# Kernel tuning notes

Measured on AMD Instinct MI355X. Metric: run time of the kernel, lower is better.

The kernel has to match this reference:

```python
import jax, jax.numpy as jnp
import numpy as np

N = 100000   # nodes
E = 800000   # edges
F_IN, H, C = 128, 128, 47
L = 3        # layers


def setup_inputs() -> dict:
    key = jax.random.key(0)
    ks = jax.random.split(key, 10)
    x = jax.random.normal(ks[0], (N, F_IN), dtype=jnp.float32)
    src = jax.random.randint(ks[1], (E,), 0, N, dtype=jnp.int32)
    dst = jax.random.randint(ks[2], (E,), 0, N, dtype=jnp.int32)
    w = jax.random.uniform(ks[3], (L, E), dtype=jnp.float32)
    W0 = jax.random.normal(ks[4], (F_IN, H), dtype=jnp.float32) * 0.05
    b0 = jnp.zeros((H,), jnp.float32)
    W1 = jax.random.normal(ks[5], (H, H), dtype=jnp.float32) * 0.05
    b1 = jnp.zeros((H,), jnp.float32)
    W2 = jax.random.normal(ks[6], (H, C), dtype=jnp.float32) * 0.05
    b2 = jnp.zeros((C,), jnp.float32)
    return {"x": x, "src": src, "dst": dst, "w": w,
            "W0": W0, "b0": b0, "W1": W1, "b1": b1, "W2": W2, "b2": b2}


def reference(x, src, dst, w, W0, b0, W1, b1, W2, b2):
    seg = lambda v, idx: jax.ops.segment_sum(v, idx, num_segments=N)
    ones = jnp.ones((src.shape[0],), x.dtype)
    # DGL GraphConv norm='both': structural degrees, clamped to >= 1
    inv_sqrt_out = jnp.maximum(seg(ones, src), 1.0) ** -0.5  # [N]
    inv_sqrt_in = jnp.maximum(seg(ones, dst), 1.0) ** -0.5   # [N]

    def gcn_layer(h, we, W, b):
        h = h * inv_sqrt_out[:, None]          # src normalization
        h = h @ W                               # linear (commutes with linear agg)
        m = h[src] * we[:, None]                # edge-weighted messages [E, d]
        agg = seg(m, dst)                       # scatter-add to dst [N, d]
        return agg * inv_sqrt_in[:, None] + b   # dst normalization + bias

    h = jax.nn.relu(gcn_layer(x, w[0], W0, b0))
    h = jax.nn.relu(gcn_layer(h, w[1], W1, b1))
    return gcn_layer(h, w[2], W2, b2)
```

## Files before the change

### kernel.cpp

```cpp
#include <hip/hip_runtime.h>


typedef short s16x8 __attribute__((ext_vector_type(8)));
typedef float f32x4 __attribute__((ext_vector_type(4)));

static constexpr int CAP = 24;

__device__ __forceinline__ unsigned short f2bf(float f) {
    unsigned int u = __float_as_uint(f);
    u += 0x7FFFu + ((u >> 16) & 1u);
    return (unsigned short)(u >> 16);
}
__device__ __forceinline__ float bf2f(unsigned short v) {
    return __uint_as_float((unsigned int)v << 16);
}

__global__ __launch_bounds__(256)
void pack_all(const float* __restrict__ W0, const float* __restrict__ W1,
              const float* __restrict__ W2, unsigned short* __restrict__ Wp) {
    int idx = blockIdx.x * 256 + threadIdx.x;
    if (idx < 32768) {
        const float* W = (idx < 16384) ? W0 : W1;
        unsigned short* D = Wp + ((idx < 16384) ? 0 : 16384);
        int i = idx & 16383;
        int k = i >> 7, col = i & 127;
        float v = W[k * 128 + col];
        int kk = k >> 5, kr = k & 31;
        int lane = ((kr >> 3) << 4) | (col & 15);
        int ct = col >> 4, j = kr & 7;
        D[(((kk * 8) + ct) * 64 + lane) * 8 + j] = f2bf(v);
    } else if (idx < 40960) {
        int i = idx - 32768;
        int k = i >> 6, col = i & 63;
        float v = (col < 47) ? W2[k * 47 + col] : 0.0f;
        int kk = k >> 5, kr = k & 31;
        int lane = ((kr >> 3) << 4) | (col & 15);
        int ct = col >> 4, j = kr & 7;
        (Wp + 32768)[(((kk * 4) + ct) * 64 + lane) * 8 + j] = f2bf(v);
    }
}

__global__ __launch_bounds__(256)
void mega_fill_gemm0(const int* __restrict__ src, const int* __restrict__ dst,
                     const float* __restrict__ w, int E,
                     int* __restrict__ dego, int* __restrict__ cursor,
                     float4* __restrict__ swb,
                     int* __restrict__ spill_cnt, int2* __restrict__ spill,
                     const float* __restrict__ x,
                     const unsigned short* __restrict__ Wp0,
                     unsigned short* __restrict__ y, int N, int gemm_blocks) {
    const int b = blockIdx.x;
    if (b % 3 == 2) {
        const int gb = b / 3;
        if (gb >= gemm_blocks) return;
        const int lane = threadIdx.x & 63;
        const int wid  = threadIdx.x >> 6;
        const int row0 = gb * 64 + wid * 16;
        const int kgrp = lane >> 4;
        const int c    = lane & 15;
        int ar = row0 + c;
        if (ar > N - 1) ar = N - 1;
        const float* xrow = &x[(size_t)ar * 128];

        f32x4 acc[8];
        #pragma unroll
        for (int ct = 0; ct < 8; ++ct) acc[ct] = {0.f, 0.f, 0.f, 0.f};

        #pragma unroll
        for (int kk = 0; kk < 4; ++kk) {
            float4 u0 = *(const float4*)&xrow[kk * 32 + kgrp * 8];
            float4 u1 = *(const float4*)&xrow[kk * 32 + kgrp * 8 + 4];
            s16x8 af;
            af[0] = (short)f2bf(u0.x); af[1] = (short)f2bf(u0.y);
            af[2] = (short)f2bf(u0.z); af[3] = (short)f2bf(u0.w);
            af[4] = (short)f2bf(u1.x); af[5] = (short)f2bf(u1.y);
            af[6] = (short)f2bf(u1.z); af[7] = (short)f2bf(u1.w);
            #pragma unroll
            for (int ct = 0; ct < 8; ++ct) {
                s16x8 bf = *(const s16x8*)&Wp0[((size_t)(kk * 8 + ct) * 64 + lane) * 8];
                acc[ct] = __builtin_amdgcn_mfma_f32_16x16x32_bf16(af, bf, acc[ct], 0, 0, 0);
            }
        }
        #pragma unroll
        for (int ct = 0; ct < 8; ++ct) {
            #pragma unroll
            for (int i = 0; i < 4; ++i) {
                int row = row0 + kgrp * 4 + i;
                if (row < N) y[(size_t)row * 128 + ct * 16 + c] = f2bf(acc[ct][i]);
            }
        }
    } else {
        const int fb = b - b / 3;
        int e = fb * 256 + (int)threadIdx.x;
        if (e >= E) return;
        int s = src[e];
        int d = dst[e];
        atomicAdd(&dego[s], 1);
        int pos = atomicAdd(&cursor[d], 1);
        if (pos < CAP) {
            swb[(size_t)d * CAP + pos] =
                make_float4(__int_as_float(s), w[e], w[E + e], w[2 * (size_t)E + e]);
        } else {
            int sp = atomicAdd(spill_cnt, 1);
            spill[sp] = make_int2(d, e);
        }
    }
}

template<int PC>
__global__ __launch_bounds__(256)
void gemm_direct(const unsigned short* __restrict__ h,
                 const unsigned short* __restrict__ Wp,
                 unsigned short* __restrict__ y, int N) {
    constexpr int CT = PC / 16;
    const int lane = threadIdx.x & 63;
    const int wid  = threadIdx.x >> 6;
    const int row0 = blockIdx.x * 64 + wid * 16;
    const int kgrp = lane >> 4;
    const int c    = lane & 15;

    int ar = row0 + c;
    if (ar > N - 1) ar = N - 1;
    const unsigned short* hrow = &h[(size_t)ar * 128 + kgrp * 8];

    f32x4 acc[CT];
    #pragma unroll
    for (int ct = 0; ct < CT; ++ct) acc[ct] = {0.f, 0.f, 0.f, 0.f};

    #pragma unroll
    for (int kk = 0; kk < 4; ++kk) {
        s16x8 af = *(const s16x8*)&hrow[kk * 32];
        #pragma unroll
        for (int ct = 0; ct < CT; ++ct) {
            s16x8 bf = *(const s16x8*)&Wp[((size_t)(kk * CT + ct) * 64 + lane) * 8];
            acc[ct] = __builtin_amdgcn_mfma_f32_16x16x32_bf16(af, bf, acc[ct], 0, 0, 0);
        }
    }

    #pragma unroll
    for (int ct = 0; ct < CT; ++ct) {
        #pragma unroll
        for (int i = 0; i < 4; ++i) {
            int row = row0 + kgrp * 4 + i;
            if (row < N) y[(size_t)row * PC + ct * 16 + c] = f2bf(acc[ct][i]);
        }
    }
}

template<int PC, int WSEL, bool FINAL>
__global__ __launch_bounds__(256)
void gather_w(const unsigned short* __restrict__ yb, const float4* __restrict__ swb,
              const int* __restrict__ degi, const int* __restrict__ dego,
              const int* __restrict__ spill_cnt, const int2* __restrict__ spill,
              const int* __restrict__ src, const float* __restrict__ wl,
              const float* __restrict__ b, void* __restrict__ outp, int N) {
    constexpr int TPN = PC / 4;
    constexpr int EPG = 64 / TPN;
    const int n = blockIdx.x * 4 + (threadIdx.x >> 6);
    if (n >= N) return;
    const int t    = threadIdx.x & 63;
    const int lane = t & (TPN - 1);
    const int g    = t / TPN;

    const ushort4* yv = (const ushort4*)yb;
    const float4* rec = swb + (size_t)n * CAP;
    const int dg  = degi[n];
    const int cnt = dg < CAP ? dg : CAP;

    float a0 = 0.f, a1 = 0.f, a2 = 0.f, a3 = 0.f;
    int p = g;

#define SELW(m) ((WSEL == 0) ? (m).y : (WSEL == 1) ? (m).z : (m).w)
#define EDGE_FMA(m, v) do {                                                   \
        int _s = __float_as_int((m).x);                                       \
        int _d = dego[_s]; if (_d < 1) _d = 1;                                \
        float _w = SELW(m) * rsqrtf((float)_d);                               \
        a0 = fmaf(bf2f((v).x), _w, a0);                                       \
        a1 = fmaf(bf2f((v).y), _w, a1);                                       \
        a2 = fmaf(bf2f((v).z), _w, a2);                                       \
        a3 = fmaf(bf2f((v).w), _w, a3);                                       \
    } while (0)

    for (; p + 3 * EPG < cnt; p += 4 * EPG) {
        float4 m0 = rec[p];
        float4 m1 = rec[p + EPG];
        float4 m2 = rec[p + 2 * EPG];
        float4 m3 = rec[p + 3 * EPG];
        ushort4 v0 = yv[(size_t)__float_as_int(m0.x) * TPN + lane];
        ushort4 v1 = yv[(size_t)__float_as_int(m1.x) * TPN + lane];
        ushort4 v2 = yv[(size_t)__float_as_int(m2.x) * TPN + lane];
        ushort4 v3 = yv[(size_t)__float_as_int(m3.x) * TPN + lane];
        EDGE_FMA(m0, v0); EDGE_FMA(m1, v1); EDGE_FMA(m2, v2); EDGE_FMA(m3, v3);
    }
    for (; p + EPG < cnt; p += 2 * EPG) {
        float4 m0 = rec[p];
        float4 m1 = rec[p + EPG];
        ushort4 v0 = yv[(size_t)__float_as_int(m0.x) * TPN + lane];
        ushort4 v1 = yv[(size_t)__float_as_int(m1.x) * TPN + lane];
        EDGE_FMA(m0, v0); EDGE_FMA(m1, v1);
    }
    if (p < cnt) {
        float4 m0 = rec[p];
        ushort4 v0 = yv[(size_t)__float_as_int(m0.x) * TPN + lane];
        EDGE_FMA(m0, v0);
    }
    if (dg > CAP && g == 0) {
        int sc = *spill_cnt;
        for (int i = 0; i < sc; ++i) {
            int2 sp = spill[i];
            if (sp.x == n) {
                int e = sp.y;
                int s0 = src[e];
                int d0 = dego[s0]; if (d0 < 1) d0 = 1;
                float w0 = wl[e] * rsqrtf((float)d0);
                ushort4 v0 = yv[(size_t)s0 * TPN + lane];
                a0 = fmaf(bf2f(v0.x), w0, a0);
                a1 = fmaf(bf2f(v0.y), w0, a1);
                a2 = fmaf(bf2f(v0.z), w0, a2);
                a3 = fmaf(bf2f(v0.w), w0, a3);
            }
        }
    }
#undef EDGE_FMA
#undef SELW

    #pragma unroll
    for (int m = TPN; m < 64; m <<= 1) {
        a0 += __shfl_xor(a0, m, 64);
        a1 += __shfl_xor(a1, m, 64);
        a2 += __shfl_xor(a2, m, 64);
        a3 += __shfl_xor(a3, m, 64);
    }
    if (g != 0) return;

    const float inv = rsqrtf((float)(dg < 1 ? 1 : dg));
    if (FINAL) {
        float* out = (float*)outp;
        const int c = lane * 4;
        float aa[4] = {a0, a1, a2, a3};
        #pragma unroll
        for (int j = 0; j < 4; ++j) {
            if (c + j < 47) out[(size_t)n * 47 + c + j] = fmaf(aa[j], inv, b[c + j]);
        }
    } else {
        unsigned short* out = (unsigned short*)outp;
        float4 bb = *(const float4*)&b[lane * 4];
        float4 v;
        v.x = fmaxf(fmaf(a0, inv, bb.x), 0.f);
        v.y = fmaxf(fmaf(a1, inv, bb.y), 0.f);
        v.z = fmaxf(fmaf(a2, inv, bb.z), 0.f);
        v.w = fmaxf(fmaf(a3, inv, bb.w), 0.f);
        ushort4 o;
        o.x = f2bf(v.x); o.y = f2bf(v.y); o.z = f2bf(v.z); o.w = f2bf(v.w);
        *(ushort4*)&out[(size_t)n * PC + lane * 4] = o;
    }
}

extern "C" void kernel_launch(void* const* d_in, const int* in_sizes, int n_in,
                              void* d_out, int out_size, void* d_ws, size_t ws_size,
                              hipStream_t stream) {
    const float* x   = (const float*)d_in[0];
    const int*   src = (const int*)d_in[1];
    const int*   dst = (const int*)d_in[2];
    const float* w   = (const float*)d_in[3];
    const float* W0  = (const float*)d_in[4];
    const float* b0  = (const float*)d_in[5];
    const float* W1  = (const float*)d_in[6];
    const float* b1  = (const float*)d_in[7];
    const float* W2  = (const float*)d_in[8];
    const float* b2  = (const float*)d_in[9];

    const int N = in_sizes[0] / 128;
    const int E = in_sizes[1];

    char* p = (char*)d_ws;
    unsigned short* xh = (unsigned short*)p; p += (size_t)N * 128 * sizeof(unsigned short);
    unsigned short* y  = (unsigned short*)p; p += (size_t)N * 128 * sizeof(unsigned short);
    float4* swb    = (float4*)p; p += (size_t)N * CAP * sizeof(float4);
    int2*   spill  = (int2*)p;   p += (size_t)E * sizeof(int2);
    unsigned short* Wp = (unsigned short*)p; p += (size_t)(16384 * 2 + 8192) * sizeof(unsigned short);
    int*   dego    = (int*)p;    p += (size_t)N * sizeof(int);
    int*   cursor  = (int*)p;    p += (size_t)N * sizeof(int);
    int*   spill_cnt = (int*)p;  p += 4 * sizeof(int);

    unsigned short* Wp1 = Wp + 16384;
    unsigned short* Wp2 = Wp + 32768;

    hipMemsetAsync(dego, 0, (2 * (size_t)N + 4) * sizeof(int), stream);
    pack_all<<<160, 256, 0, stream>>>(W0, W1, W2, Wp);

    const int gemm_blocks = (N + 63) / 64;
    const int fill_blocks = (E + 255) / 256;
    int grid = 3 * gemm_blocks;
    if (grid - grid / 3 < fill_blocks) grid = (3 * fill_blocks + 1) / 2 + 2;
    mega_fill_gemm0<<<grid, 256, 0, stream>>>(
        src, dst, w, E, dego, cursor, swb, spill_cnt, spill,
        x, Wp, y, N, gemm_blocks);

    const int gather_blocks = (N + 3) / 4;

    gather_w<128, 0, false><<<gather_blocks, 256, 0, stream>>>(
        y, swb, cursor, dego, spill_cnt, spill, src, w, b0, xh, N);

    gemm_direct<128><<<gemm_blocks, 256, 0, stream>>>(xh, Wp1, y, N);
    gather_w<128, 1, false><<<gather_blocks, 256, 0, stream>>>(
        y, swb, cursor, dego, spill_cnt, spill, src, w + E, b1, xh, N);

    gemm_direct<64><<<gemm_blocks, 256, 0, stream>>>(xh, Wp2, y, N);
    gather_w<64, 2, true><<<gather_blocks, 256, 0, stream>>>(
        y, swb, cursor, dego, spill_cnt, spill, src, w + 2 * (size_t)E, b2, d_out, N);
}
```

Before: 255.0 us.

## Fuse gather with next-layer GEMM via LDS; shrink edge records to (src, edge id)

Each layer's gather/aggregate is fused with the following layer's MFMA GEMM. Every block aggregates 64 destination rows into swizzled shared memory and then runs the GEMM from LDS, so the intermediate bf16 activations never make a round trip through global memory and two launches go away. Edge records shrink from float4 (src plus three weights) to uint2 (src, edge id). The weight is now gathered per edge from the layer's weight array, which adds an indirect load in exchange for a smaller fill write and record read. The fused kernel drops from 64 to 32 lanes per node and processes its 16 rows per wave sequentially, which lowers parallelism and the number of loads in flight.

```diff
diff --git a/kernel.cpp b/kernel.cpp
--- a/kernel.cpp
+++ b/kernel.cpp
@@ -42,9 +42,9 @@
 
 __global__ __launch_bounds__(256)
 void mega_fill_gemm0(const int* __restrict__ src, const int* __restrict__ dst,
-                     const float* __restrict__ w, int E,
+                     int E,
                      int* __restrict__ dego, int* __restrict__ cursor,
-                     float4* __restrict__ swb,
+                     uint2* __restrict__ swe,
                      int* __restrict__ spill_cnt, int2* __restrict__ spill,
                      const float* __restrict__ x,
                      const unsigned short* __restrict__ Wp0,
@@ -98,8 +98,8 @@
         atomicAdd(&dego[s], 1);
         int pos = atomicAdd(&cursor[d], 1);
         if (pos < CAP) {
-            swb[(size_t)d * CAP + pos] =
-                make_float4(__int_as_float(s), w[e], w[E + e], w[2 * (size_t)E + e]);
+            uint2 r; r.x = (unsigned)s; r.y = (unsigned)e;
+            swe[(size_t)d * CAP + pos] = r;
         } else {
             int sp = atomicAdd(spill_cnt, 1);
             spill[sp] = make_int2(d, e);
@@ -107,21 +107,93 @@
     }
 }
 
-template<int PC>
+template<int PCOUT>
 __global__ __launch_bounds__(256)
-void gemm_direct(const unsigned short* __restrict__ h,
-                 const unsigned short* __restrict__ Wp,
-                 unsigned short* __restrict__ y, int N) {
-    constexpr int CT = PC / 16;
+void fused_gather_gemm(const unsigned short* __restrict__ yin,
+                       const uint2* __restrict__ swe,
+                       const int* __restrict__ degi, const int* __restrict__ dego,
+                       const int* __restrict__ spill_cnt, const int2* __restrict__ spill,
+                       const int* __restrict__ srcA, const float* __restrict__ wl,
+                       const float* __restrict__ bv,
+                       const unsigned short* __restrict__ Wp,
+                       unsigned short* __restrict__ yout, int N) {
+    constexpr int CT = PCOUT / 16;
+    __shared__ unsigned short hs[64 * 128];
     const int lane = threadIdx.x & 63;
     const int wid  = threadIdx.x >> 6;
     const int row0 = blockIdx.x * 64 + wid * 16;
+    if (row0 >= N) return;
+    const int l = lane & 31;
+    const int g = lane >> 5;
+    const ushort4* yv = (const ushort4*)yin;
+
+    float4 bb = *(const float4*)&bv[l * 4];
+
+#define EFMA(rr) do {                                                         \
+        float _w = wl[(rr).y];                                                \
+        int _d = dego[(rr).x]; if (_d < 1) _d = 1;                            \
+        ushort4 _v = yv[(size_t)(rr).x * 32 + l];                             \
+        _w *= rsqrtf((float)_d);                                              \
+        a0 = fmaf(bf2f(_v.x), _w, a0);                                        \
+        a1 = fmaf(bf2f(_v.y), _w, a1);                                        \
+        a2 = fmaf(bf2f(_v.z), _w, a2);                                        \
+        a3 = fmaf(bf2f(_v.w), _w, a3);                                        \
+    } while (0)
+
+    #pragma unroll 1
+    for (int i = 0; i < 16; ++i) {
+        const int n  = row0 + i;
+        const int rl = wid * 16 + i;
+        const unsigned swz = (unsigned)((rl & 7) << 4);
+        if (n < N) {
+            const uint2* rec = swe + (size_t)n * CAP;
+            const int dg  = degi[n];
+            const int cnt = dg < CAP ? dg : CAP;
+            float a0 = 0.f, a1 = 0.f, a2 = 0.f, a3 = 0.f;
+            int p = g;
+            for (; p + 2 < cnt; p += 4) {
+                uint2 r0 = rec[p];
+                uint2 r1 = rec[p + 2];
+                EFMA(r0); EFMA(r1);
+            }
+            if (p < cnt) {
+                uint2 r0 = rec[p];
+                EFMA(r0);
+            }
+            if (dg > CAP && g == 0) {
+                int sc = *spill_cnt;
+                for (int q = 0; q < sc; ++q) {
+                    int2 sp = spill[q];
+                    if (sp.x == n) {
+                        uint2 r0; r0.x = (unsigned)srcA[sp.y]; r0.y = (unsigned)sp.y;
+                        EFMA(r0);
+                    }
+                }
+            }
+            a0 += __shfl_xor(a0, 32, 64);
+            a1 += __shfl_xor(a1, 32, 64);
+            a2 += __shfl_xor(a2, 32, 64);
+            a3 += __shfl_xor(a3, 32, 64);
+            if (g == 0) {
+                const float inv = rsqrtf((float)(dg < 1 ? 1 : dg));
+                ushort4 o;
+                o.x = f2bf(fmaxf(fmaf(a0, inv, bb.x), 0.f));
+                o.y = f2bf(fmaxf(fmaf(a1, inv, bb.y), 0.f));
+                o.z = f2bf(fmaxf(fmaf(a2, inv, bb.z), 0.f));
+                o.w = f2bf(fmaxf(fmaf(a3, inv, bb.w), 0.f));
+                *(ushort4*)((char*)hs + rl * 256 + ((unsigned)(l * 8) ^ swz)) = o;
+            }
+        } else if (g == 0) {
+            ushort4 o; o.x = 0; o.y = 0; o.z = 0; o.w = 0;
+            *(ushort4*)((char*)hs + rl * 256 + ((unsigned)(l * 8) ^ swz)) = o;
+        }
+    }
+#undef EFMA
+
     const int kgrp = lane >> 4;
     const int c    = lane & 15;
-
-    int ar = row0 + c;
-    if (ar > N - 1) ar = N - 1;
-    const unsigned short* hrow = &h[(size_t)ar * 128 + kgrp * 8];
+    const int arl  = wid * 16 + c;
+    const unsigned aswz = (unsigned)((arl & 7) << 4);
 
     f32x4 acc[CT];
     #pragma unroll
@@ -129,7 +201,8 @@
 
     #pragma unroll
     for (int kk = 0; kk < 4; ++kk) {
-        s16x8 af = *(const s16x8*)&hrow[kk * 32];
+        s16x8 af = *(const s16x8*)((const char*)hs + arl * 256 +
+                                   ((unsigned)(kk * 64 + kgrp * 16) ^ aswz));
         #pragma unroll
         for (int ct = 0; ct < CT; ++ct) {
             s16x8 bf = *(const s16x8*)&Wp[((size_t)(kk * CT + ct) * 64 + lane) * 8];
@@ -142,117 +215,79 @@
         #pragma unroll
         for (int i = 0; i < 4; ++i) {
             int row = row0 + kgrp * 4 + i;
-            if (row < N) y[(size_t)row * PC + ct * 16 + c] = f2bf(acc[ct][i]);
-        }
-    }
-}
-
-template<int PC, int WSEL, bool FINAL>
+            if (row < N) yout[(size_t)row * PCOUT + ct * 16 + c] = f2bf(acc[ct][i]);
+        }
+    }
+}
+
 __global__ __launch_bounds__(256)
-void gather_w(const unsigned short* __restrict__ yb, const float4* __restrict__ swb,
-              const int* __restrict__ degi, const int* __restrict__ dego,
-              const int* __restrict__ spill_cnt, const int2* __restrict__ spill,
-              const int* __restrict__ src, const float* __restrict__ wl,
-              const float* __restrict__ b, void* __restrict__ outp, int N) {
-    constexpr int TPN = PC / 4;
-    constexpr int EPG = 64 / TPN;
+void gather_final(const unsigned short* __restrict__ yin,
+                  const uint2* __restrict__ swe,
+                  const int* __restrict__ degi, const int* __restrict__ dego,
+                  const int* __restrict__ spill_cnt, const int2* __restrict__ spill,
+                  const int* __restrict__ srcA, const float* __restrict__ wl,
+                  const float* __restrict__ bv, float* __restrict__ out, int N) {
     const int n = blockIdx.x * 4 + (threadIdx.x >> 6);
     if (n >= N) return;
-    const int t    = threadIdx.x & 63;
-    const int lane = t & (TPN - 1);
-    const int g    = t / TPN;
-
-    const ushort4* yv = (const ushort4*)yb;
-    const float4* rec = swb + (size_t)n * CAP;
+    const int t = threadIdx.x & 63;
+    const int l = t & 15;
+    const int g = t >> 4;
+    const ushort4* yv = (const ushort4*)yin;
+
+    const uint2* rec = swe + (size_t)n * CAP;
     const int dg  = degi[n];
     const int cnt = dg < CAP ? dg : CAP;
-
     float a0 = 0.f, a1 = 0.f, a2 = 0.f, a3 = 0.f;
+
+#define EFMA(rr) do {                                                         \
+        float _w = wl[(rr).y];                                                \
+        int _d = dego[(rr).x]; if (_d < 1) _d = 1;                            \
+        ushort4 _v = yv[(size_t)(rr).x * 16 + l];                             \
+        _w *= rsqrtf((float)_d);                                              \
+        a0 = fmaf(bf2f(_v.x), _w, a0);                                        \
+        a1 = fmaf(bf2f(_v.y), _w, a1);                                        \
+        a2 = fmaf(bf2f(_v.z), _w, a2);                                        \
+        a3 = fmaf(bf2f(_v.w), _w, a3);                                        \
+    } while (0)
+
     int p = g;
-
-#define SELW(m) ((WSEL == 0) ? (m).y : (WSEL == 1) ? (m).z : (m).w)
-#define EDGE_FMA(m, v) do {                                                   \
-        int _s = __float_as_int((m).x);                                       \
-        int _d = dego[_s]; if (_d < 1) _d = 1;                                \
-        float _w = SELW(m) * rsqrtf((float)_d);                               \
-        a0 = fmaf(bf2f((v).x), _w, a0);                                       \
-        a1 = fmaf(bf2f((v).y), _w, a1);                                       \
-        a2 = fmaf(bf2f((v).z), _w, a2);                                       \
-        a3 = fmaf(bf2f((v).w), _w, a3);                                       \
-    } while (0)
-
-    for (; p + 3 * EPG < cnt; p += 4 * EPG) {
-        float4 m0 = rec[p];
-        float4 m1 = rec[p + EPG];
-        float4 m2 = rec[p + 2 * EPG];
-        float4 m3 = rec[p + 3 * EPG];
-        ushort4 v0 = yv[(size_t)__float_as_int(m0.x) * TPN + lane];
-        ushort4 v1 = yv[(size_t)__float_as_int(m1.x) * TPN + lane];
-        ushort4 v2 = yv[(size_t)__float_as_int(m2.x) * TPN + lane];
-        ushort4 v3 = yv[(size_t)__float_as_int(m3.x) * TPN + lane];
-        EDGE_FMA(m0, v0); EDGE_FMA(m1, v1); EDGE_FMA(m2, v2); EDGE_FMA(m3, v3);
-    }
-    for (; p + EPG < cnt; p += 2 * EPG) {
-        float4 m0 = rec[p];
-        float4 m1 = rec[p + EPG];
-        ushort4 v0 = yv[(size_t)__float_as_int(m0.x) * TPN + lane];
-        ushort4 v1 = yv[(size_t)__float_as_int(m1.x) * TPN + lane];
-        EDGE_FMA(m0, v0); EDGE_FMA(m1, v1);
+    for (; p + 4 < cnt; p += 8) {
+        uint2 r0 = rec[p];
+        uint2 r1 = rec[p + 4];
+        EFMA(r0); EFMA(r1);
     }
     if (p < cnt) {
-        float4 m0 = rec[p];
-        ushort4 v0 = yv[(size_t)__float_as_int(m0.x) * TPN + lane];
-        EDGE_FMA(m0, v0);
+        uint2 r0 = rec[p];
+        EFMA(r0);
     }
     if (dg > CAP && g == 0) {
         int sc = *spill_cnt;
-        for (int i = 0; i < sc; ++i) {
-            int2 sp = spill[i];
+        for (int q = 0; q < sc; ++q) {
+            int2 sp = spill[q];
             if (sp.x == n) {
-                int e = sp.y;
-                int s0 = src[e];
-                int d0 = dego[s0]; if (d0 < 1) d0 = 1;
-                float w0 = wl[e] * rsqrtf((float)d0);
-                ushort4 v0 = yv[(size_t)s0 * TPN + lane];
-                a0 = fmaf(bf2f(v0.x), w0, a0);
-                a1 = fmaf(bf2f(v0.y), w0, a1);
-                a2 = fmaf(bf2f(v0.z), w0, a2);
-                a3 = fmaf(bf2f(v0.w), w0, a3);
-            }
-        }
-    }
-#undef EDGE_FMA
-#undef SELW
-
+                uint2 r0; r0.x = (unsigned)srcA[sp.y]; r0.y = (unsigned)sp.y;
+                EFMA(r0);
+            }
+        }
+    }
+#undef EFMA
+
+    a0 += __shfl_xor(a0, 16, 64);
+    a1 += __shfl_xor(a1, 16, 64);
+    a2 += __shfl_xor(a2, 16, 64);
+    a3 += __shfl_xor(a3, 16, 64);
+    a0 += __shfl_xor(a0, 32, 64);
+    a1 += __shfl_xor(a1, 32, 64);
+    a2 += __shfl_xor(a2, 32, 64);
+    a3 += __shfl_xor(a3, 32, 64);
+    if (g != 0) return;
+
+    const float inv = rsqrtf((float)(dg < 1 ? 1 : dg));
+    const int c = l * 4;
+    float aa[4] = {a0, a1, a2, a3};
     #pragma unroll
-    for (int m = TPN; m < 64; m <<= 1) {
-        a0 += __shfl_xor(a0, m, 64);
-        a1 += __shfl_xor(a1, m, 64);
-        a2 += __shfl_xor(a2, m, 64);
-        a3 += __shfl_xor(a3, m, 64);
-    }
-    if (g != 0) return;
-
-    const float inv = rsqrtf((float)(dg < 1 ? 1 : dg));
-    if (FINAL) {
-        float* out = (float*)outp;
-        const int c = lane * 4;
-        float aa[4] = {a0, a1, a2, a3};
-        #pragma unroll
-        for (int j = 0; j < 4; ++j) {
-            if (c + j < 47) out[(size_t)n * 47 + c + j] = fmaf(aa[j], inv, b[c + j]);
-        }
-    } else {
-        unsigned short* out = (unsigned short*)outp;
-        float4 bb = *(const float4*)&b[lane * 4];
-        float4 v;
-        v.x = fmaxf(fmaf(a0, inv, bb.x), 0.f);
-        v.y = fmaxf(fmaf(a1, inv, bb.y), 0.f);
-        v.z = fmaxf(fmaf(a2, inv, bb.z), 0.f);
-        v.w = fmaxf(fmaf(a3, inv, bb.w), 0.f);
-        ushort4 o;
-        o.x = f2bf(v.x); o.y = f2bf(v.y); o.z = f2bf(v.z); o.w = f2bf(v.w);
-        *(ushort4*)&out[(size_t)n * PC + lane * 4] = o;
+    for (int j = 0; j < 4; ++j) {
+        if (c + j < 47) out[(size_t)n * 47 + c + j] = fmaf(aa[j], inv, bv[c + j]);
     }
 }
 
@@ -274,10 +309,11 @@
     const int E = in_sizes[1];
 
     char* p = (char*)d_ws;
-    unsigned short* xh = (unsigned short*)p; p += (size_t)N * 128 * sizeof(unsigned short);
-    unsigned short* y  = (unsigned short*)p; p += (size_t)N * 128 * sizeof(unsigned short);
-    float4* swb    = (float4*)p; p += (size_t)N * CAP * sizeof(float4);
-    int2*   spill  = (int2*)p;   p += (size_t)E * sizeof(int2);
+    unsigned short* yA = (unsigned short*)p; p += (size_t)N * 128 * sizeof(unsigned short);
+    unsigned short* yB = (unsigned short*)p; p += (size_t)N * 128 * sizeof(unsigned short);
+    unsigned short* yC = (unsigned short*)p; p += (size_t)N * 64 * sizeof(unsigned short);
+    uint2* swe     = (uint2*)p;  p += (size_t)N * CAP * sizeof(uint2);
+    int2*  spill   = (int2*)p;   p += (size_t)E * sizeof(int2);
     unsigned short* Wp = (unsigned short*)p; p += (size_t)(16384 * 2 + 8192) * sizeof(unsigned short);
     int*   dego    = (int*)p;    p += (size_t)N * sizeof(int);
     int*   cursor  = (int*)p;    p += (size_t)N * sizeof(int);
@@ -294,19 +330,14 @@
     int grid = 3 * gemm_blocks;
     if (grid - grid / 3 < fill_blocks) grid = (3 * fill_blocks + 1) / 2 + 2;
     mega_fill_gemm0<<<grid, 256, 0, stream>>>(
-        src, dst, w, E, dego, cursor, swb, spill_cnt, spill,
-        x, Wp, y, N, gemm_blocks);
-
-    const int gather_blocks = (N + 3) / 4;
-
-    gather_w<128, 0, false><<<gather_blocks, 256, 0, stream>>>(
-        y, swb, cursor, dego, spill_cnt, spill, src, w, b0, xh, N);
-
-    gemm_direct<128><<<gemm_blocks, 256, 0, stream>>>(xh, Wp1, y, N);
-    gather_w<128, 1, false><<<gather_blocks, 256, 0, stream>>>(
-        y, swb, cursor, dego, spill_cnt, spill, src, w + E, b1, xh, N);
-
-    gemm_direct<64><<<gemm_blocks, 256, 0, stream>>>(xh, Wp2, y, N);
-    gather_w<64, 2, true><<<gather_blocks, 256, 0, stream>>>(
-        y, swb, cursor, dego, spill_cnt, spill, src, w + 2 * (size_t)E, b2, d_out, N);
-}
+        src, dst, E, dego, cursor, swe, spill_cnt, spill, x, Wp, yA, N, gemm_blocks);
+
+    fused_gather_gemm<128><<<gemm_blocks, 256, 0, stream>>>(
+        yA, swe, cursor, dego, spill_cnt, spill, src, w, b0, Wp1, yB, N);
+    fused_gather_gemm<64><<<gemm_blocks, 256, 0, stream>>>(
+        yB, swe, cursor, dego, spill_cnt, spill, src, w + E, b1, Wp2, yC, N);
+
+    gather_final<<<(N + 3) / 4, 256, 0, stream>>>(
+        yC, swe, cursor, dego, spill_cnt, spill, src, w + 2 * (size_t)E, b2,
+        (float*)d_out, N);
+}
```

Result: slower. 287.8 us (+12.9%).

## Fuse whole GCN pipeline into one cooperative persistent kernel with grid syncs

Applied to the files above, without the earlier changes.

Replaces the memset plus seven separate kernel launches with a single cooperative persistent kernel. Each phase (init, edge fill, three GEMMs, three gathers) runs as a grid-stride loop over a grid capped at 1024 blocks, with grid.sync between phases. The aim is to remove launch overhead and inter-kernel gaps. The trade-offs are the loss of overlap between fill and GEMM0, the cost of seven grid barriers, and the limited grid size, which may underuse latency hiding in the gather phases. Edge record stores also become nontemporal, and a multi-kernel fallback is kept.

```diff
diff --git a/kernel.cpp b/kernel.cpp
--- a/kernel.cpp
+++ b/kernel.cpp
@@ -1,4 +1,7 @@
 #include <hip/hip_runtime.h>
+#include <hip/hip_cooperative_groups.h>
+
+namespace cg = cooperative_groups;
 
 
 typedef short s16x8 __attribute__((ext_vector_type(8)));
@@ -15,165 +18,142 @@
     return __uint_as_float((unsigned int)v << 16);
 }
 
-__global__ __launch_bounds__(256)
-void pack_all(const float* __restrict__ W0, const float* __restrict__ W1,
-              const float* __restrict__ W2, unsigned short* __restrict__ Wp) {
-    int idx = blockIdx.x * 256 + threadIdx.x;
-    if (idx < 32768) {
-        const float* W = (idx < 16384) ? W0 : W1;
-        unsigned short* D = Wp + ((idx < 16384) ? 0 : 16384);
-        int i = idx & 16383;
-        int k = i >> 7, col = i & 127;
-        float v = W[k * 128 + col];
-        int kk = k >> 5, kr = k & 31;
-        int lane = ((kr >> 3) << 4) | (col & 15);
-        int ct = col >> 4, j = kr & 7;
-        D[(((kk * 8) + ct) * 64 + lane) * 8 + j] = f2bf(v);
-    } else if (idx < 40960) {
-        int i = idx - 32768;
-        int k = i >> 6, col = i & 63;
-        float v = (col < 47) ? W2[k * 47 + col] : 0.0f;
-        int kk = k >> 5, kr = k & 31;
-        int lane = ((kr >> 3) << 4) | (col & 15);
-        int ct = col >> 4, j = kr & 7;
-        (Wp + 32768)[(((kk * 4) + ct) * 64 + lane) * 8 + j] = f2bf(v);
-    }
-}
-
-__global__ __launch_bounds__(256)
-void mega_fill_gemm0(const int* __restrict__ src, const int* __restrict__ dst,
-                     const float* __restrict__ w, int E,
-                     int* __restrict__ dego, int* __restrict__ cursor,
-                     float4* __restrict__ swb,
-                     int* __restrict__ spill_cnt, int2* __restrict__ spill,
-                     const float* __restrict__ x,
-                     const unsigned short* __restrict__ Wp0,
-                     unsigned short* __restrict__ y, int N, int gemm_blocks) {
-    const int b = blockIdx.x;
-    if (b % 3 == 2) {
-        const int gb = b / 3;
-        if (gb >= gemm_blocks) return;
-        const int lane = threadIdx.x & 63;
-        const int wid  = threadIdx.x >> 6;
-        const int row0 = gb * 64 + wid * 16;
-        const int kgrp = lane >> 4;
-        const int c    = lane & 15;
-        int ar = row0 + c;
-        if (ar > N - 1) ar = N - 1;
-        const float* xrow = &x[(size_t)ar * 128];
-
-        f32x4 acc[8];
-        #pragma unroll
-        for (int ct = 0; ct < 8; ++ct) acc[ct] = {0.f, 0.f, 0.f, 0.f};
-
-        #pragma unroll
-        for (int kk = 0; kk < 4; ++kk) {
+struct GcnP {
+    const int*   src;
+    const int*   dst;
+    const float* w;
+    const float* x;
+    const float* W0; const float* b0;
+    const float* W1; const float* b1;
+    const float* W2; const float* b2;
+    unsigned short* Wp;
+    unsigned short* xh;
+    unsigned short* y;
+    float4* swb;
+    int2*   spill;
+    int*    dego;
+    int*    cursor;
+    int*    spill_cnt;
+    float*  out;
+    int N, E;
+};
+
+__device__ __forceinline__ void phase_init(const GcnP& p, int gtid, int gsz) {
+    for (int i = gtid; i < 2 * p.N + 4; i += gsz) p.dego[i] = 0;
+    for (int idx = gtid; idx < 40960; idx += gsz) {
+        if (idx < 32768) {
+            const float* W = (idx < 16384) ? p.W0 : p.W1;
+            unsigned short* D = p.Wp + ((idx < 16384) ? 0 : 16384);
+            int i = idx & 16383;
+            int k = i >> 7, col = i & 127;
+            float v = W[k * 128 + col];
+            int kk = k >> 5, kr = k & 31;
+            int ln = ((kr >> 3) << 4) | (col & 15);
+            int ct = col >> 4, j = kr & 7;
+            D[(((kk * 8) + ct) * 64 + ln) * 8 + j] = f2bf(v);
+        } else {
+            int i = idx - 32768;
+            int k = i >> 6, col = i & 63;
+            float v = (col < 47) ? p.W2[k * 47 + col] : 0.0f;
+            int kk = k >> 5, kr = k & 31;
+            int ln = ((kr >> 3) << 4) | (col & 15);
+            int ct = col >> 4, j = kr & 7;
+            (p.Wp + 32768)[(((kk * 4) + ct) * 64 + ln) * 8 + j] = f2bf(v);
+        }
+    }
+}
+
+__device__ __forceinline__ void phase_fill(const GcnP& p, int gtid, int gsz) {
+    for (int e = gtid; e < p.E; e += gsz) {
+        int s = p.src[e];
+        int d = p.dst[e];
+        atomicAdd(&p.dego[s], 1);
+        int pos = atomicAdd(&p.cursor[d], 1);
+        if (pos < CAP) {
+            f32x4 r = { __int_as_float(s), p.w[e], p.w[p.E + e],
+                        p.w[2 * (size_t)p.E + e] };
+            __builtin_nontemporal_store(r, (f32x4*)&p.swb[(size_t)d * CAP + pos]);
+        } else {
+            int sp = atomicAdd(p.spill_cnt, 1);
+            p.spill[sp] = make_int2(d, e);
+        }
+    }
+}
+
+template<int PC, bool F32IN>
+__device__ __forceinline__ void gemm_tile(int row0, const void* hvoid,
+        const unsigned short* Wp, unsigned short* y, int N, int lane, int wid) {
+    constexpr int CT = PC / 16;
+    const int r0   = row0 + wid * 16;
+    const int kgrp = lane >> 4;
+    const int c    = lane & 15;
+    int ar = r0 + c;
+    if (ar > N - 1) ar = N - 1;
+
+    f32x4 acc[CT];
+    #pragma unroll
+    for (int ct = 0; ct < CT; ++ct) acc[ct] = {0.f, 0.f, 0.f, 0.f};
+
+    #pragma unroll
+    for (int kk = 0; kk < 4; ++kk) {
+        s16x8 af;
+        if (F32IN) {
+            const float* xrow = (const float*)hvoid + (size_t)ar * 128;
             float4 u0 = *(const float4*)&xrow[kk * 32 + kgrp * 8];
             float4 u1 = *(const float4*)&xrow[kk * 32 + kgrp * 8 + 4];
-            s16x8 af;
             af[0] = (short)f2bf(u0.x); af[1] = (short)f2bf(u0.y);
             af[2] = (short)f2bf(u0.z); af[3] = (short)f2bf(u0.w);
             af[4] = (short)f2bf(u1.x); af[5] = (short)f2bf(u1.y);
             af[6] = (short)f2bf(u1.z); af[7] = (short)f2bf(u1.w);
-            #pragma unroll
-            for (int ct = 0; ct < 8; ++ct) {
-                s16x8 bf = *(const s16x8*)&Wp0[((size_t)(kk * 8 + ct) * 64 + lane) * 8];
-                acc[ct] = __builtin_amdgcn_mfma_f32_16x16x32_bf16(af, bf, acc[ct], 0, 0, 0);
-            }
-        }
-        #pragma unroll
-        for (int ct = 0; ct < 8; ++ct) {
-            #pragma unroll
-            for (int i = 0; i < 4; ++i) {
-                int row = row0 + kgrp * 4 + i;
-                if (row < N) y[(size_t)row * 128 + ct * 16 + c] = f2bf(acc[ct][i]);
-            }
-        }
-    } else {
-        const int fb = b - b / 3;
-        int e = fb * 256 + (int)threadIdx.x;
-        if (e >= E) return;
-        int s = src[e];
-        int d = dst[e];
-        atomicAdd(&dego[s], 1);
-        int pos = atomicAdd(&cursor[d], 1);
-        if (pos < CAP) {
-            swb[(size_t)d * CAP + pos] =
-                make_float4(__int_as_float(s), w[e], w[E + e], w[2 * (size_t)E + e]);
         } else {
-            int sp = atomicAdd(spill_cnt, 1);
-            spill[sp] = make_int2(d, e);
-        }
-    }
-}
-
-template<int PC>
-__global__ __launch_bounds__(256)
-void gemm_direct(const unsigned short* __restrict__ h,
-                 const unsigned short* __restrict__ Wp,
-                 unsigned short* __restrict__ y, int N) {
-    constexpr int CT = PC / 16;
-    const int lane = threadIdx.x & 63;
-    const int wid  = threadIdx.x >> 6;
-    const int row0 = blockIdx.x * 64 + wid * 16;
-    const int kgrp = lane >> 4;
-    const int c    = lane & 15;
-
-    int ar = row0 + c;
-    if (ar > N - 1) ar = N - 1;
-    const unsigned short* hrow = &h[(size_t)ar * 128 + kgrp * 8];
-
-    f32x4 acc[CT];
-    #pragma unroll
-    for (int ct = 0; ct < CT; ++ct) acc[ct] = {0.f, 0.f, 0.f, 0.f};
-
-    #pragma unroll
-    for (int kk = 0; kk < 4; ++kk) {
-        s16x8 af = *(const s16x8*)&hrow[kk * 32];
+            const unsigned short* hrow =
+                (const unsigned short*)hvoid + (size_t)ar * 128 + kgrp * 8;
+            af = *(const s16x8*)&hrow[kk * 32];
+        }
         #pragma unroll
         for (int ct = 0; ct < CT; ++ct) {
             s16x8 bf = *(const s16x8*)&Wp[((size_t)(kk * CT + ct) * 64 + lane) * 8];
             acc[ct] = __builtin_amdgcn_mfma_f32_16x16x32_bf16(af, bf, acc[ct], 0, 0, 0);
         }
     }
-
     #pragma unroll
     for (int ct = 0; ct < CT; ++ct) {
         #pragma unroll
         for (int i = 0; i < 4; ++i) {
-            int row = row0 + kgrp * 4 + i;
+            int row = r0 + kgrp * 4 + i;
             if (row < N) y[(size_t)row * PC + ct * 16 + c] = f2bf(acc[ct][i]);
         }
     }
 }
 
+template<int PC, bool F32IN>
+__device__ __forceinline__ void phase_gemm(const GcnP& p, const void* h,
+        const unsigned short* Wp, int bid, int nb, int lane, int wid) {
+    const int tiles = (p.N + 63) >> 6;
+    for (int tb = bid; tb < tiles; tb += nb)
+        gemm_tile<PC, F32IN>(tb * 64, h, Wp, p.y, p.N, lane, wid);
+}
+
 template<int PC, int WSEL, bool FINAL>
-__global__ __launch_bounds__(256)
-void gather_w(const unsigned short* __restrict__ yb, const float4* __restrict__ swb,
-              const int* __restrict__ degi, const int* __restrict__ dego,
-              const int* __restrict__ spill_cnt, const int2* __restrict__ spill,
-              const int* __restrict__ src, const float* __restrict__ wl,
-              const float* __restrict__ b, void* __restrict__ outp, int N) {
+__device__ __forceinline__ void gather_node(const GcnP& p,
+        const unsigned short* yb, const float* bvec, void* outp, int n, int t) {
     constexpr int TPN = PC / 4;
     constexpr int EPG = 64 / TPN;
-    const int n = blockIdx.x * 4 + (threadIdx.x >> 6);
-    if (n >= N) return;
-    const int t    = threadIdx.x & 63;
     const int lane = t & (TPN - 1);
     const int g    = t / TPN;
 
     const ushort4* yv = (const ushort4*)yb;
-    const float4* rec = swb + (size_t)n * CAP;
-    const int dg  = degi[n];
+    const float4* rec = p.swb + (size_t)n * CAP;
+    const int dg  = p.cursor[n];
     const int cnt = dg < CAP ? dg : CAP;
 
     float a0 = 0.f, a1 = 0.f, a2 = 0.f, a3 = 0.f;
-    int p = g;
+    int q = g;
 
 #define SELW(m) ((WSEL == 0) ? (m).y : (WSEL == 1) ? (m).z : (m).w)
 #define EDGE_FMA(m, v) do {                                                   \
         int _s = __float_as_int((m).x);                                       \
-        int _d = dego[_s]; if (_d < 1) _d = 1;                                \
+        int _d = p.dego[_s]; if (_d < 1) _d = 1;                              \
         float _w = SELW(m) * rsqrtf((float)_d);                               \
         a0 = fmaf(bf2f((v).x), _w, a0);                                       \
         a1 = fmaf(bf2f((v).y), _w, a1);                                       \
@@ -181,37 +161,38 @@
         a3 = fmaf(bf2f((v).w), _w, a3);                                       \
     } while (0)
 
-    for (; p + 3 * EPG < cnt; p += 4 * EPG) {
-        float4 m0 = rec[p];
-        float4 m1 = rec[p + EPG];
-        float4 m2 = rec[p + 2 * EPG];
-        float4 m3 = rec[p + 3 * EPG];
+    for (; q + 3 * EPG < cnt; q += 4 * EPG) {
+        float4 m0 = rec[q];
+        float4 m1 = rec[q + EPG];
+        float4 m2 = rec[q + 2 * EPG];
+        float4 m3 = rec[q + 3 * EPG];
         ushort4 v0 = yv[(size_t)__float_as_int(m0.x) * TPN + lane];
         ushort4 v1 = yv[(size_t)__float_as_int(m1.x) * TPN + lane];
         ushort4 v2 = yv[(size_t)__float_as_int(m2.x) * TPN + lane];
         ushort4 v3 = yv[(size_t)__float_as_int(m3.x) * TPN + lane];
         EDGE_FMA(m0, v0); EDGE_FMA(m1, v1); EDGE_FMA(m2, v2); EDGE_FMA(m3, v3);
     }
-    for (; p + EPG < cnt; p += 2 * EPG) {
-        float4 m0 = rec[p];
-        float4 m1 = rec[p + EPG];
+    for (; q + EPG < cnt; q += 2 * EPG) {
+        float4 m0 = rec[q];
+        float4 m1 = rec[q + EPG];
         ushort4 v0 = yv[(size_t)__float_as_int(m0.x) * TPN + lane];
         ushort4 v1 = yv[(size_t)__float_as_int(m1.x) * TPN + lane];
         EDGE_FMA(m0, v0); EDGE_FMA(m1, v1);
     }
-    if (p < cnt) {
-        float4 m0 = rec[p];
+    if (q < cnt) {
+        float4 m0 = rec[q];
         ushort4 v0 = yv[(size_t)__float_as_int(m0.x) * TPN + lane];
         EDGE_FMA(m0, v0);
     }
     if (dg > CAP && g == 0) {
-        int sc = *spill_cnt;
+        const float* wl = p.w + (size_t)WSEL * p.E;
+        int sc = *p.spill_cnt;
         for (int i = 0; i < sc; ++i) {
-            int2 sp = spill[i];
+            int2 sp = p.spill[i];
             if (sp.x == n) {
                 int e = sp.y;
-                int s0 = src[e];
-                int d0 = dego[s0]; if (d0 < 1) d0 = 1;
+                int s0 = p.src[e];
+                int d0 = p.dego[s0]; if (d0 < 1) d0 = 1;
                 float w0 = wl[e] * rsqrtf((float)d0);
                 ushort4 v0 = yv[(size_t)s0 * TPN + lane];
                 a0 = fmaf(bf2f(v0.x), w0, a0);
@@ -231,45 +212,102 @@
         a2 += __shfl_xor(a2, m, 64);
         a3 += __shfl_xor(a3, m, 64);
     }
-    if (g != 0) return;
-
-    const float inv = rsqrtf((float)(dg < 1 ? 1 : dg));
-    if (FINAL) {
-        float* out = (float*)outp;
-        const int c = lane * 4;
-        float aa[4] = {a0, a1, a2, a3};
-        #pragma unroll
-        for (int j = 0; j < 4; ++j) {
-            if (c + j < 47) out[(size_t)n * 47 + c + j] = fmaf(aa[j], inv, b[c + j]);
-        }
-    } else {
-        unsigned short* out = (unsigned short*)outp;
-        float4 bb = *(const float4*)&b[lane * 4];
-        float4 v;
-        v.x = fmaxf(fmaf(a0, inv, bb.x), 0.f);
-        v.y = fmaxf(fmaf(a1, inv, bb.y), 0.f);
-        v.z = fmaxf(fmaf(a2, inv, bb.z), 0.f);
-        v.w = fmaxf(fmaf(a3, inv, bb.w), 0.f);
-        ushort4 o;
-        o.x = f2bf(v.x); o.y = f2bf(v.y); o.z = f2bf(v.z); o.w = f2bf(v.w);
-        *(ushort4*)&out[(size_t)n * PC + lane * 4] = o;
-    }
+    if (g == 0) {
+        const float inv = rsqrtf((float)(dg < 1 ? 1 : dg));
+        if (FINAL) {
+            float* out = (float*)outp;
+            const int c = lane * 4;
+            float aa[4] = {a0, a1, a2, a3};
+            #pragma unroll
+            for (int j = 0; j < 4; ++j) {
+                if (c + j < 47) out[(size_t)n * 47 + c + j] = fmaf(aa[j], inv, bvec[c + j]);
+            }
+        } else {
+            unsigned short* out = (unsigned short*)outp;
+            float4 bb = *(const float4*)&bvec[lane * 4];
+            float4 v;
+            v.x = fmaxf(fmaf(a0, inv, bb.x), 0.f);
+            v.y = fmaxf(fmaf(a1, inv, bb.y), 0.f);
+            v.z = fmaxf(fmaf(a2, inv, bb.z), 0.f);
+            v.w = fmaxf(fmaf(a3, inv, bb.w), 0.f);
+            ushort4 o;
+            o.x = f2bf(v.x); o.y = f2bf(v.y); o.z = f2bf(v.z); o.w = f2bf(v.w);
+            *(ushort4*)&out[(size_t)n * PC + lane * 4] = o;
+        }
+    }
+}
+
+template<int PC, int WSEL, bool FINAL>
+__device__ __forceinline__ void phase_gather(const GcnP& p, const float* bvec,
+        void* outp, int gw, int nwv, int lane) {
+    for (int n = gw; n < p.N; n += nwv)
+        gather_node<PC, WSEL, FINAL>(p, p.y, bvec, outp, n, lane);
+}
+
+__global__ __launch_bounds__(256)
+void gcn_all(GcnP p) {
+    cg::grid_group grid = cg::this_grid();
+    const int tid  = threadIdx.x;
+    const int bid  = blockIdx.x;
+    const int nb   = gridDim.x;
+    const int gtid = bid * 256 + tid;
+    const int gsz  = nb * 256;
+    const int lane = tid & 63;
+    const int wid  = tid >> 6;
+    const int gw   = bid * 4 + wid;
+    const int nwv  = nb * 4;
+
+    phase_init(p, gtid, gsz);
+    grid.sync();
+    phase_fill(p, gtid, gsz);
+    grid.sync();
+    phase_gemm<128, true>(p, p.x, p.Wp, bid, nb, lane, wid);
+    grid.sync();
+    phase_gather<128, 0, false>(p, p.b0, p.xh, gw, nwv, lane);
+    grid.sync();
+    phase_gemm<128, false>(p, p.xh, p.Wp + 16384, bid, nb, lane, wid);
+    grid.sync();
+    phase_gather<128, 1, false>(p, p.b1, p.xh, gw, nwv, lane);
+    grid.sync();
+    phase_gemm<64, false>(p, p.xh, p.Wp + 32768, bid, nb, lane, wid);
+    grid.sync();
+    phase_gather<64, 2, true>(p, p.b2, p.out, gw, nwv, lane);
+}
+
+__global__ __launch_bounds__(256) void k_init(GcnP p) {
+    phase_init(p, blockIdx.x * 256 + threadIdx.x, gridDim.x * 256);
+}
+__global__ __launch_bounds__(256) void k_fill(GcnP p) {
+    phase_fill(p, blockIdx.x * 256 + threadIdx.x, gridDim.x * 256);
+}
+__global__ __launch_bounds__(256) void k_gemm0(GcnP p) {
+    phase_gemm<128, true>(p, p.x, p.Wp, blockIdx.x, gridDim.x,
+                          threadIdx.x & 63, threadIdx.x >> 6);
+}
+__global__ __launch_bounds__(256) void k_gemm1(GcnP p) {
+    phase_gemm<128, false>(p, p.xh, p.Wp + 16384, blockIdx.x, gridDim.x,
+                           threadIdx.x & 63, threadIdx.x >> 6);
+}
+__global__ __launch_bounds__(256) void k_gemm2(GcnP p) {
+    phase_gemm<64, false>(p, p.xh, p.Wp + 32768, blockIdx.x, gridDim.x,
+                          threadIdx.x & 63, threadIdx.x >> 6);
+}
+__global__ __launch_bounds__(256) void k_gather0(GcnP p) {
+    phase_gather<128, 0, false>(p, p.b0, p.xh,
+        blockIdx.x * 4 + (threadIdx.x >> 6), gridDim.x * 4, threadIdx.x & 63);
+}
+__global__ __launch_bounds__(256) void k_gather1(GcnP p) {
+    phase_gather<128, 1, false>(p, p.b1, p.xh,
+        blockIdx.x * 4 + (threadIdx.x >> 6), gridDim.x * 4, threadIdx.x & 63);
+}
+__global__ __launch_bounds__(256) void k_gather2(GcnP p) {
+    phase_gather<64, 2, true>(p, p.b2, p.out,
+        blockIdx.x * 4 + (threadIdx.x >> 6), gridDim.x * 4, threadIdx.x & 63);
 }
 
 extern "C" void kernel_launch(void* const* d_in, const int* in_sizes, int n_in,
                               void* d_out, int out_size, void* d_ws, size_t ws_size,
                               hipStream_t stream) {
-    const float* x   = (const float*)d_in[0];
-    const int*   src = (const int*)d_in[1];
-    const int*   dst = (const int*)d_in[2];
-    const float* w   = (const float*)d_in[3];
-    const float* W0  = (const float*)d_in[4];
-    const float* b0  = (const float*)d_in[5];
-    const float* W1  = (const float*)d_in[6];
-    const float* b1  = (const float*)d_in[7];
-    const float* W2  = (const float*)d_in[8];
-    const float* b2  = (const float*)d_in[9];
-
     const int N = in_sizes[0] / 128;
     const int E = in_sizes[1];
 
@@ -279,34 +317,59 @@
     float4* swb    = (float4*)p; p += (size_t)N * CAP * sizeof(float4);
     int2*   spill  = (int2*)p;   p += (size_t)E * sizeof(int2);
     unsigned short* Wp = (unsigned short*)p; p += (size_t)(16384 * 2 + 8192) * sizeof(unsigned short);
-    int*   dego    = (int*)p;    p += (size_t)N * sizeof(int);
-    int*   cursor  = (int*)p;    p += (size_t)N * sizeof(int);
-    int*   spill_cnt = (int*)p;  p += 4 * sizeof(int);
-
-    unsigned short* Wp1 = Wp + 16384;
-    unsigned short* Wp2 = Wp + 32768;
-
-    hipMemsetAsync(dego, 0, (2 * (size_t)N + 4) * sizeof(int), stream);
-    pack_all<<<160, 256, 0, stream>>>(W0, W1, W2, Wp);
-
-    const int gemm_blocks = (N + 63) / 64;
-    const int fill_blocks = (E + 255) / 256;
-    int grid = 3 * gemm_blocks;
-    if (grid - grid / 3 < fill_blocks) grid = (3 * fill_blocks + 1) / 2 + 2;
-    mega_fill_gemm0<<<grid, 256, 0, stream>>>(
-        src, dst, w, E, dego, cursor, swb, spill_cnt, spill,
-        x, Wp, y, N, gemm_blocks);
-
-    const int gather_blocks = (N + 3) / 4;
-
-    gather_w<128, 0, false><<<gather_blocks, 256, 0, stream>>>(
-        y, swb, cursor, dego, spill_cnt, spill, src, w, b0, xh, N);
-
-    gemm_direct<128><<<gemm_blocks, 256, 0, stream>>>(xh, Wp1, y, N);
-    gather_w<128, 1, false><<<gather_blocks, 256, 0, stream>>>(
-        y, swb, cursor, dego, spill_cnt, spill, src, w + E, b1, xh, N);
-
-    gemm_direct<64><<<gemm_blocks, 256, 0, stream>>>(xh, Wp2, y, N);
-    gather_w<64, 2, true><<<gather_blocks, 256, 0, stream>>>(
-        y, swb, cursor, dego, spill_cnt, spill, src, w + 2 * (size_t)E, b2, d_out, N);
-}
+    int*    dego   = (int*)p;    p += (size_t)N * sizeof(int);
+    int*    cursor = (int*)p;    p += (size_t)N * sizeof(int);
+    int*    spill_cnt = (int*)p; p += 4 * sizeof(int);
+
+    GcnP prm;
+    prm.src = (const int*)d_in[1];
+    prm.dst = (const int*)d_in[2];
+    prm.w   = (const float*)d_in[3];
+    prm.x   = (const float*)d_in[0];
+    prm.W0  = (const float*)d_in[4];  prm.b0 = (const float*)d_in[5];
+    prm.W1  = (const float*)d_in[6];  prm.b1 = (const float*)d_in[7];
+    prm.W2  = (const float*)d_in[8];  prm.b2 = (const float*)d_in[9];
+    prm.Wp  = Wp;
+    prm.xh  = xh;
+    prm.y   = y;
+    prm.swb = swb;
+    prm.spill = spill;
+    prm.dego = dego;
+    prm.cursor = cursor;
+    prm.spill_cnt = spill_cnt;
+    prm.out = (float*)d_out;
+    prm.N = N;
+    prm.E = E;
+
+    int dev = 0;
+    (void)hipGetDevice(&dev);
+    int numCU = 0;
+    (void)hipDeviceGetAttribute(&numCU, hipDeviceAttributeMultiprocessorCount, dev);
+    int maxPerCU = 0;
+    hipError_t oe = hipOccupancyMaxActiveBlocksPerMultiprocessor(
+        &maxPerCU, (const void*)gcn_all, 256, 0);
+
+    bool done = false;
+    if (oe == hipSuccess && numCU > 0 && maxPerCU > 0) {
+        int grid = maxPerCU * numCU;
+        if (grid > 1024) grid = 1024;
+        if (grid >= 256) {
+            void* args[] = { (void*)&prm };
+            hipError_t le = hipLaunchCooperativeKernel(
+                (void*)gcn_all, dim3(grid), dim3(256), args, 0, stream);
+            done = (le == hipSuccess);
+        }
+    }
+
+    if (!done) {
+        const int zblocks = (2 * N + 4 + 255) / 256;
+        k_init<<<zblocks, 256, 0, stream>>>(prm);
+        k_fill<<<(E + 255) / 256, 256, 0, stream>>>(prm);
+        k_gemm0<<<(N + 63) / 64, 256, 0, stream>>>(prm);
+        k_gather0<<<(N + 3) / 4, 256, 0, stream>>>(prm);
+        k_gemm1<<<(N + 63) / 64, 256, 0, stream>>>(prm);
+        k_gather1<<<(N + 3) / 4, 256, 0, stream>>>(prm);
+        k_gemm2<<<(N + 63) / 64, 256, 0, stream>>>(prm);
+        k_gather2<<<(N + 3) / 4, 256, 0, stream>>>(prm);
+    }
+}
```

Result: slower. 1.004 ms (+293.9%).
